# Kernel tuning notes

Hardware: AMD Instinct MI355X
Metric: run time of the kernel (lower is better)

Reference implementation:

```python
import jax, jax.numpy as jnp
import numpy as np

DT = 0.5
DX = 0.01
MU_UP = 4e-05
PAD = 3  # 7x7 kernel // 2

_LAP = np.array([[0, 0, 0, 2, 0, 0, 0],
                 [0, 0, 0, -27, 0, 0, 0],
                 [0, 0, 0, 270, 0, 0, 0],
                 [2, -27, 270, -980, 270, -27, 2],
                 [0, 0, 0, 270, 0, 0, 0],
                 [0, 0, 0, -27, 0, 0, 0],
                 [0, 0, 0, 2, 0, 0, 0]], dtype=np.float32)
LAP_W = jnp.asarray(_LAP / (DX * DX) / 180.0)[None, None]  # [1,1,7,7]


def _laplace(x):
    # x: [B,1,H,W]; circular padding then valid conv (matches padding_mode='circular')
    xp = jnp.pad(x, ((0, 0), (0, 0), (PAD, PAD), (PAD, PAD)), mode='wrap')
    return jax.lax.conv_general_dilated(xp, LAP_W, (1, 1), 'VALID',
                                        dimension_numbers=('NCHW', 'OIHW', 'NCHW'))


def setup_inputs() -> dict:
    key = jax.random.key(0)
    ks = jax.random.split(key, 7)
    h = jax.random.uniform(ks[0], (16, 2, 1024, 1024), dtype=jnp.float32)
    CA = jax.random.uniform(ks[1], (), dtype=jnp.float32) - 0.5  # ~ -rand()+0.5
    CB = jax.random.uniform(ks[2], (), dtype=jnp.float32) - 0.5
    NA = -jax.random.uniform(ks[3], (), dtype=jnp.float32)
    NB = jax.random.uniform(ks[4], (), dtype=jnp.float32)
    f = 0.1 * jax.random.uniform(ks[5], (), dtype=jnp.float32)
    k = 0.1 * jax.random.uniform(ks[6], (), dtype=jnp.float32)
    return {"h": h, "CA": CA, "CB": CB, "NA": NA, "NB": NB, "f": f, "k": k}


def reference(h, CA, CB, NA, NB, f, k):
    mu_u = MU_UP * jax.nn.sigmoid(CA)
    mu_v = MU_UP * jax.nn.sigmoid(CB)

    def f_rhs(u, v):
        uv2 = u * v * v
        f_u = mu_u * _laplace(u) + NA * uv2 + f * (1.0 - u)
        f_v = mu_v * _laplace(v) + NB * uv2 - (k + f) * v
        return f_u, f_v

    u0 = h[:, 0:1]
    v0 = h[:, 1:2]
    k1_u, k1_v = f_rhs(u0, v0)
    k2_u, k2_v = f_rhs(u0 + k1_u * (DT / 2.0), v0 + k1_v * (DT / 2.0))
    k3_u, k3_v = f_rhs(u0 + k2_u * (DT / 2.0), v0 + k2_v * (DT / 2.0))
    k4_u, k4_v = f_rhs(u0 + k3_u * DT, v0 + k3_v * DT)
    u_next = u0 + DT * (k1_u + 2.0 * k2_u + 2.0 * k3_u + k4_u) / 6.0
    v_next = v0 + DT * (k1_v + 2.0 * k2_v + 2.0 * k3_v + k4_v) / 6.0
    return jnp.concatenate((u_next, v_next), axis=1)
```

## Files before the change

### kernel.cpp

```cpp
#include <hip/hip_runtime.h>


typedef float f2 __attribute__((ext_vector_type(2)));

#define HROWS 64
#define NT    512
#define STEPS (HROWS + 24)

#define W0 ((-980.0f / 1e-4f) / 180.0f)
#define W1 ((  270.0f / 1e-4f) / 180.0f)
#define W2 (( -27.0f / 1e-4f) / 180.0f)
#define W3 ((   2.0f / 1e-4f) / 180.0f)

__device__ __forceinline__ f2 sp(float s) { f2 r; r.x = s; r.y = s; return r; }
__device__ __forceinline__ f2 pfma(float s, f2 a, f2 c) {
    return __builtin_elementwise_fma(sp(s), a, c);
}

__device__ __forceinline__ unsigned pk2(f2 a) {
    unsigned ua = __float_as_uint(a.x), ub = __float_as_uint(a.y);
    return ((ua + 0x8000u) >> 16) | ((ub + 0x8000u) & 0xffff0000u);
}
__device__ __forceinline__ float bhi(unsigned d) { return __uint_as_float(d); }
__device__ __forceinline__ float blo(unsigned d) { return __uint_as_float(d << 16); }

__device__ __forceinline__ void evalp7x(f2 w0, f2 w1, f2 w2, f2 w3, f2 w4,
                                        f2 w5, f2 w6, f2 m1, f2 p1,
                                        float am3, float bp3,
                                        f2& lap, f2& ctr)
{
    ctr = w3;
    f2 vp = pfma(W1, w2 + w4, pfma(W2, w1 + w5, sp(W3) * (w0 + w6)));
    f2 m1q; m1q.x = m1.y;  m1q.y = ctr.x;
    f2 p1q; p1q.x = ctr.y; p1q.y = p1.x;
    f2 m3q; m3q.x = am3;   m3q.y = m1.x;
    f2 p3q; p3q.x = p1.y;  p3q.y = bp3;
    f2 hp = pfma(W1, m1q + p1q, pfma(W2, m1 + p1, sp(W3) * (m3q + p3q)));
    lap = pfma(W0, ctr, hp + vp);
}

__global__ __launch_bounds__(NT, 1) void rcnn_rk4_march(
    const float* __restrict__ h,
    const float* __restrict__ pCA, const float* __restrict__ pCB,
    const float* __restrict__ pNA, const float* __restrict__ pNB,
    const float* __restrict__ pf,  const float* __restrict__ pk,
    float* __restrict__ out)
{
    __shared__ uint2 S[4][4][NT];

    const int tid = threadIdx.x;
    const int Y0  = blockIdx.x * HROWS;
    const int b   = blockIdx.z;

    const float NA = pNA[0], NB = pNB[0];
    const float ff = pf[0];
    const float kpf = pk[0] + pf[0];
    const float mu_u = 4e-5f / (1.0f + expf(-pCA[0]));
    const float mu_v = 4e-5f / (1.0f + expf(-pCB[0]));

    const size_t baseU = (size_t)b * 2u * 1048576u;
    const size_t baseV = baseU + 1048576u;
    const float* hU = h + baseU + 2 * tid;
    const float* hV = h + baseV + 2 * tid;
    float* oU = out + baseU + 2 * tid;
    float* oV = out + baseV + 2 * tid;

    const int xm2 = (tid - 2) & 511;
    const int xm1 = (tid - 1) & 511;
    const int xp1 = (tid + 1) & 511;
    const int xp2 = (tid + 2) & 511;

    f2 Uu[8], Uv[8], Du[8], Dv[8];
    f2 Y1u[8], Y1v[8], Y2u[8], Y2v[8], Y3u[8], Y3v[8];
    f2 ACu[8], ACv[8];

    const f2 z = sp(0.0f);
    #pragma unroll
    for (int j = 0; j < 8; ++j) {
        Uu[j]=z; Uv[j]=z; Du[j]=z; Dv[j]=z;
        Y1u[j]=z; Y1v[j]=z; Y2u[j]=z; Y2v[j]=z; Y3u[j]=z; Y3v[j]=z;
        ACu[j]=z; ACv[j]=z;
    }

    f2 pAu, pAv, pBu, pBv;
    {
        int r0 = (Y0 - 12) & 1023;
        int r1 = (Y0 - 11) & 1023;
        pAu = *(const f2*)(hU + (size_t)r0 * 1024);
        pAv = *(const f2*)(hV + (size_t)r0 * 1024);
        pBu = *(const f2*)(hU + (size_t)r1 * 1024);
        pBv = *(const f2*)(hV + (size_t)r1 * 1024);
    }

#define NBR(sidx, cc)                                                         \
      const uint2* Ls = &S[sidx][((cc)+2)&3][0];                              \
      uint2 m2d = Ls[xm2], m1d = Ls[xm1], p1d = Ls[xp1], p2d = Ls[xp2];       \
      f2 m1u; m1u.x = blo(m1d.x); m1u.y = bhi(m1d.x);                         \
      f2 p1u; p1u.x = blo(p1d.x); p1u.y = bhi(p1d.x);                         \
      f2 m1v; m1v.x = blo(m1d.y); m1v.y = bhi(m1d.y);                         \
      f2 p1v; p1v.x = blo(p1d.y); p1v.y = bhi(p1d.y);                         \
      float am3u = bhi(m2d.x), am3v = bhi(m2d.y);                             \
      float bp3u = blo(p2d.x), bp3v = blo(p2d.y);

#define STEP(c, G1, G2, G3, G4, tb_)                                          \
  {                                                                           \
    const int t_ = (tb_) + (c);                                               \
                             \
    Du[(c)&7] = Uu[((c)+3)&7]; Dv[(c)&7] = Uv[((c)+3)&7];                     \
                                             \
    Uu[(c)&7] = ((c)&1) ? pBu : pAu;                                          \
    Uv[(c)&7] = ((c)&1) ? pBv : pAv;                                          \
             \
    S[0][(c)&3][tid] = make_uint2(pk2(Uu[((c)+7)&7]), pk2(Uv[((c)+7)&7]));    \
                                             \
    {                                                                         \
      int yn = (Y0 - 10 + t_) & 1023;                                         \
      f2 au = *(const f2*)(hU + (size_t)yn * 1024);                           \
      f2 av = *(const f2*)(hV + (size_t)yn * 1024);                           \
      if ((c)&1) { pBu = au; pBv = av; } else { pAu = au; pAv = av; }         \
    }                                                                         \
    if (G1) {                                         \
      NBR(0, c)                                                               \
      f2 lU, cU, lV, cV;                                                      \
      evalp7x(Uu[((c)+2)&7], Uu[((c)+3)&7], Uu[((c)+4)&7], Uu[((c)+5)&7],     \
              Uu[((c)+6)&7], Uu[((c)+7)&7], Uu[(c)&7],                        \
              m1u, p1u, am3u, bp3u, lU, cU);                                  \
      evalp7x(Uv[((c)+2)&7], Uv[((c)+3)&7], Uv[((c)+4)&7], Uv[((c)+5)&7],     \
              Uv[((c)+6)&7], Uv[((c)+7)&7], Uv[(c)&7],                        \
              m1v, p1v, am3v, bp3v, lV, cV);                                  \
      f2 uv2 = cU * cV * cV;                                                  \
      f2 kU = pfma(mu_u, lU, pfma(NA, uv2, pfma(-ff, cU, sp(ff))));           \
      f2 kV = pfma(mu_v, lV, pfma(NB, uv2, sp(-kpf) * cV));                   \
      Y1u[(c)&7] = pfma(0.25f, kU, cU);                                       \
      Y1v[(c)&7] = pfma(0.25f, kV, cV);                                       \
      S[1][(c)&3][tid] = make_uint2(pk2(Y1u[((c)+7)&7]), pk2(Y1v[((c)+7)&7]));\
    }                                                                         \
    if (G2) {                               \
      NBR(1, c)                                                               \
      f2 lU, cU, lV, cV;                                                      \
      evalp7x(Y1u[((c)+2)&7], Y1u[((c)+3)&7], Y1u[((c)+4)&7], Y1u[((c)+5)&7], \
              Y1u[((c)+6)&7], Y1u[((c)+7)&7], Y1u[(c)&7],                     \
              m1u, p1u, am3u, bp3u, lU, cU);                                  \
      evalp7x(Y1v[((c)+2)&7], Y1v[((c)+3)&7], Y1v[((c)+4)&7], Y1v[((c)+5)&7], \
              Y1v[((c)+6)&7], Y1v[((c)+7)&7], Y1v[(c)&7],                     \
              m1v, p1v, am3v, bp3v, lV, cV);                                  \
      f2 uv2 = cU * cV * cV;                                                  \
      f2 kU = pfma(mu_u, lU, pfma(NA, uv2, pfma(-ff, cU, sp(ff))));           \
      f2 kV = pfma(mu_v, lV, pfma(NB, uv2, sp(-kpf) * cV));                   \
      f2 bu = Du[((c)+7)&7], bv = Dv[((c)+7)&7];                \
      f2 nu = pfma(0.25f, kU, bu), nv = pfma(0.25f, kV, bv);                  \
      Y2u[(c)&7] = nu; Y2v[(c)&7] = nv;                                       \
      f2 aU = pfma(4.0f, Y1u[((c)+5)&7], sp(8.0f) * nu);                      \
      f2 aV = pfma(4.0f, Y1v[((c)+5)&7], sp(8.0f) * nv);                      \
      ACu[(c)&7] = pfma(-4.0f, bu, aU);                                       \
      ACv[(c)&7] = pfma(-4.0f, bv, aV);                                       \
      S[2][(c)&3][tid] = make_uint2(pk2(Y2u[((c)+7)&7]), pk2(Y2v[((c)+7)&7]));\
    }                                                                         \
    if (G3) {                                         \
      NBR(2, c)                                                               \
      f2 lU, cU, lV, cV;                                                      \
      evalp7x(Y2u[((c)+2)&7], Y2u[((c)+3)&7], Y2u[((c)+4)&7], Y2u[((c)+5)&7], \
              Y2u[((c)+6)&7], Y2u[((c)+7)&7], Y2u[(c)&7],                     \
              m1u, p1u, am3u, bp3u, lU, cU);                                  \
      evalp7x(Y2v[((c)+2)&7], Y2v[((c)+3)&7], Y2v[((c)+4)&7], Y2v[((c)+5)&7], \
              Y2v[((c)+6)&7], Y2v[((c)+7)&7], Y2v[(c)&7],                     \
              m1v, p1v, am3v, bp3v, lV, cV);                                  \
      f2 uv2 = cU * cV * cV;                                                  \
      f2 kU = pfma(mu_u, lU, pfma(NA, uv2, pfma(-ff, cU, sp(ff))));           \
      f2 kV = pfma(mu_v, lV, pfma(NB, uv2, sp(-kpf) * cV));                   \
      Y3u[(c)&7] = pfma(0.5f, kU, Du[((c)+4)&7]);               \
      Y3v[(c)&7] = pfma(0.5f, kV, Dv[((c)+4)&7]);                             \
      S[3][(c)&3][tid] = make_uint2(pk2(Y3u[((c)+7)&7]), pk2(Y3v[((c)+7)&7]));\
    }                                                                         \
    if (G4) {                         \
      NBR(3, c)                                                               \
      f2 lU, cU4, lV, cV4;                                                    \
      evalp7x(Y3u[((c)+2)&7], Y3u[((c)+3)&7], Y3u[((c)+4)&7], Y3u[((c)+5)&7], \
              Y3u[((c)+6)&7], Y3u[((c)+7)&7], Y3u[(c)&7],                     \
              m1u, p1u, am3u, bp3u, lU, cU4);                                 \
      evalp7x(Y3v[((c)+2)&7], Y3v[((c)+3)&7], Y3v[((c)+4)&7], Y3v[((c)+5)&7], \
              Y3v[((c)+6)&7], Y3v[((c)+7)&7], Y3v[(c)&7],                     \
              m1v, p1v, am3v, bp3v, lV, cV4);                                 \
      f2 uv2 = cU4 * cV4 * cV4;                                               \
      f2 kU = pfma(mu_u, lU, pfma(NA, uv2, pfma(-ff, cU4, sp(ff))));          \
      f2 kV = pfma(mu_v, lV, pfma(NB, uv2, sp(-kpf) * cV4));                  \
      f2 sU = pfma(4.0f, cU4, kU) + ACu[((c)+2)&7];             \
      f2 sV = pfma(4.0f, cV4, kV) + ACv[((c)+2)&7];                           \
      f2 oUq = sp(1.0f / 12.0f) * sU;                                         \
      f2 oVq = sp(1.0f / 12.0f) * sV;                                         \
      int yS = Y0 + t_ - 24;                                                  \
      *(f2*)(oU + (size_t)yS * 1024) = oUq;                                   \
      *(f2*)(oV + (size_t)yS * 1024) = oVq;                                   \
    }                                                                         \
    if ((c) & 1) {                                                            \
      asm volatile("s_waitcnt lgkmcnt(0)" ::: "memory");                      \
      __builtin_amdgcn_s_barrier();                                           \
    }                                                                         \
  }

    STEP(0,0,0,0,0, 0) STEP(1,0,0,0,0, 0) STEP(2,0,0,0,0, 0) STEP(3,0,0,0,0, 0)
    STEP(4,0,0,0,0, 0) STEP(5,0,0,0,0, 0) STEP(6,1,0,0,0, 0) STEP(7,1,0,0,0, 0)

    STEP(0,1,0,0,0, 8) STEP(1,1,0,0,0, 8) STEP(2,1,0,0,0, 8) STEP(3,1,0,0,0, 8)
    STEP(4,1,1,0,0, 8) STEP(5,1,1,0,0, 8) STEP(6,1,1,0,0, 8) STEP(7,1,1,0,0, 8)

    STEP(0,1,1,0,0,16) STEP(1,1,1,0,0,16) STEP(2,1,1,1,0,16) STEP(3,1,1,1,0,16)
    STEP(4,1,1,1,0,16) STEP(5,1,1,1,0,16) STEP(6,1,1,1,0,16) STEP(7,1,1,1,0,16)

    #pragma unroll 1
    for (int tb = 24; tb < STEPS; tb += 8) {
        STEP(0,1,1,1,1,tb) STEP(1,1,1,1,1,tb) STEP(2,1,1,1,1,tb) STEP(3,1,1,1,1,tb)
        STEP(4,1,1,1,1,tb) STEP(5,1,1,1,1,tb) STEP(6,1,1,1,1,tb) STEP(7,1,1,1,1,tb)
    }
#undef STEP
#undef NBR
}

extern "C" void kernel_launch(void* const* d_in, const int* in_sizes, int n_in,
                              void* d_out, int out_size, void* d_ws, size_t ws_size,
                              hipStream_t stream) {
    const float* h   = (const float*)d_in[0];
    const float* pCA = (const float*)d_in[1];
    const float* pCB = (const float*)d_in[2];
    const float* pNA = (const float*)d_in[3];
    const float* pNB = (const float*)d_in[4];
    const float* pf  = (const float*)d_in[5];
    const float* pk  = (const float*)d_in[6];
    float* outp = (float*)d_out;

    dim3 grid(1024 / HROWS, 1, 16);
    dim3 block(NT);
    rcnn_rk4_march<<<grid, block, 0, stream>>>(h, pCA, pCB, pNA, pNB, pf, pk, outp);
}
```

Baseline: 104.1 us.

## Share neighbor columns via DPP and store fp32 halos in shared memory

```diff
diff --git a/kernel.cpp b/kernel.cpp
--- a/kernel.cpp
+++ b/kernel.cpp
@@ -2,6 +2,7 @@
 
 
 typedef float f2 __attribute__((ext_vector_type(2)));
+typedef float f4 __attribute__((ext_vector_type(4)));
 
 #define HROWS 64
 #define NT    512
@@ -12,17 +13,18 @@
 #define W2 (( -27.0f / 1e-4f) / 180.0f)
 #define W3 ((   2.0f / 1e-4f) / 180.0f)
 
+#define DPP_PAIR 0xB1
+
 __device__ __forceinline__ f2 sp(float s) { f2 r; r.x = s; r.y = s; return r; }
 __device__ __forceinline__ f2 pfma(float s, f2 a, f2 c) {
     return __builtin_elementwise_fma(sp(s), a, c);
 }
 
-__device__ __forceinline__ unsigned pk2(f2 a) {
-    unsigned ua = __float_as_uint(a.x), ub = __float_as_uint(a.y);
-    return ((ua + 0x8000u) >> 16) | ((ub + 0x8000u) & 0xffff0000u);
-}
-__device__ __forceinline__ float bhi(unsigned d) { return __uint_as_float(d); }
-__device__ __forceinline__ float blo(unsigned d) { return __uint_as_float(d << 16); }
+template<int C>
+__device__ __forceinline__ float dppf(float x) {
+    return __int_as_float(__builtin_amdgcn_update_dpp(
+        0, __float_as_int(x), C, 0xF, 0xF, false));
+}
 
 __device__ __forceinline__ void evalp7x(f2 w0, f2 w1, f2 w2, f2 w3, f2 w4,
                                         f2 w5, f2 w6, f2 m1, f2 p1,
@@ -46,7 +48,7 @@
     const float* __restrict__ pf,  const float* __restrict__ pk,
     float* __restrict__ out)
 {
-    __shared__ uint2 S[4][4][NT];
+    __shared__ f4 S[4][4][NT];
 
     const int tid = threadIdx.x;
     const int Y0  = blockIdx.x * HROWS;
@@ -65,10 +67,9 @@
     float* oU = out + baseU + 2 * tid;
     float* oV = out + baseV + 2 * tid;
 
-    const int xm2 = (tid - 2) & 511;
-    const int xm1 = (tid - 1) & 511;
-    const int xp1 = (tid + 1) & 511;
-    const int xp2 = (tid + 2) & 511;
+    const bool odd = (tid & 1);
+    const int ad1 = (tid + (odd ? 1 : -1)) & 511;
+    const int ad2 = (tid + (odd ? 2 : -2)) & 511;
 
     f2 Uu[8], Uv[8], Du[8], Dv[8];
     f2 Y1u[8], Y1v[8], Y2u[8], Y2v[8], Y3u[8], Y3v[8];
@@ -92,15 +93,21 @@
         pBv = *(const f2*)(hV + (size_t)r1 * 1024);
     }
 
-#define NBR(sidx, cc)                                                         \
-      const uint2* Ls = &S[sidx][((cc)+2)&3][0];                              \
-      uint2 m2d = Ls[xm2], m1d = Ls[xm1], p1d = Ls[xp1], p2d = Ls[xp2];       \
-      f2 m1u; m1u.x = blo(m1d.x); m1u.y = bhi(m1d.x);                         \
-      f2 p1u; p1u.x = blo(p1d.x); p1u.y = bhi(p1d.x);                         \
-      f2 m1v; m1v.x = blo(m1d.y); m1v.y = bhi(m1d.y);                         \
-      f2 p1v; p1v.x = blo(p1d.y); p1v.y = bhi(p1d.y);                         \
-      float am3u = bhi(m2d.x), am3v = bhi(m2d.y);                             \
-      float bp3u = blo(p2d.x), bp3v = blo(p2d.y);
+#define NBR(Wu_, Wv_, sidx, cc)                                               \
+      const f4* Ls = &S[sidx][((cc)+2)&3][0];                                 \
+      f4 Aq = Ls[ad1];                                                        \
+      f4 Bq = Ls[ad2];                                                        \
+      f2 w3u_ = Wu_[((cc)+5)&7], w3v_ = Wv_[((cc)+5)&7];                      \
+      f2 wpu; wpu.x = dppf<DPP_PAIR>(w3u_.x); wpu.y = dppf<DPP_PAIR>(w3u_.y); \
+      f2 wpv; wpv.x = dppf<DPP_PAIR>(w3v_.x); wpv.y = dppf<DPP_PAIR>(w3v_.y); \
+      float pAux = dppf<DPP_PAIR>(Aq.x), pAuy = dppf<DPP_PAIR>(Aq.y);         \
+      float pAvx = dppf<DPP_PAIR>(Aq.z), pAvy = dppf<DPP_PAIR>(Aq.w);         \
+      f2 Au_; Au_.x = Aq.x; Au_.y = Aq.y;                                     \
+      f2 Av_; Av_.x = Aq.z; Av_.y = Aq.w;                                     \
+      f2 m1u = odd ? wpu : Au_;  f2 p1u = odd ? Au_ : wpu;                    \
+      f2 m1v = odd ? wpv : Av_;  f2 p1v = odd ? Av_ : wpv;                    \
+      float am3u = odd ? pAuy : Bq.y,  bp3u = odd ? Bq.x : pAux;              \
+      float am3v = odd ? pAvy : Bq.w,  bp3v = odd ? Bq.z : pAvx;
 
 #define STEP(c, G1, G2, G3, G4, tb_)                                          \
   {                                                                           \
@@ -110,8 +117,9 @@
                                              \
     Uu[(c)&7] = ((c)&1) ? pBu : pAu;                                          \
     Uv[(c)&7] = ((c)&1) ? pBv : pAv;                                          \
-             \
-    S[0][(c)&3][tid] = make_uint2(pk2(Uu[((c)+7)&7]), pk2(Uv[((c)+7)&7]));    \
+                          \
+    S[0][(c)&3][tid] = __builtin_shufflevector(Uu[((c)+7)&7], Uv[((c)+7)&7],  \
+                                               0, 1, 2, 3);                   \
                                              \
     {                                                                         \
       int yn = (Y0 - 10 + t_) & 1023;                                         \
@@ -120,7 +128,7 @@
       if ((c)&1) { pBu = au; pBv = av; } else { pAu = au; pAv = av; }         \
     }                                                                         \
     if (G1) {                                         \
-      NBR(0, c)                                                               \
+      NBR(Uu, Uv, 0, c)                                                       \
       f2 lU, cU, lV, cV;                                                      \
       evalp7x(Uu[((c)+2)&7], Uu[((c)+3)&7], Uu[((c)+4)&7], Uu[((c)+5)&7],     \
               Uu[((c)+6)&7], Uu[((c)+7)&7], Uu[(c)&7],                        \
@@ -133,10 +141,11 @@
       f2 kV = pfma(mu_v, lV, pfma(NB, uv2, sp(-kpf) * cV));                   \
       Y1u[(c)&7] = pfma(0.25f, kU, cU);                                       \
       Y1v[(c)&7] = pfma(0.25f, kV, cV);                                       \
-      S[1][(c)&3][tid] = make_uint2(pk2(Y1u[((c)+7)&7]), pk2(Y1v[((c)+7)&7]));\
+      S[1][(c)&3][tid] = __builtin_shufflevector(Y1u[((c)+7)&7],              \
+                                                 Y1v[((c)+7)&7], 0, 1, 2, 3); \
     }                                                                         \
     if (G2) {                               \
-      NBR(1, c)                                                               \
+      NBR(Y1u, Y1v, 1, c)                                                     \
       f2 lU, cU, lV, cV;                                                      \
       evalp7x(Y1u[((c)+2)&7], Y1u[((c)+3)&7], Y1u[((c)+4)&7], Y1u[((c)+5)&7], \
               Y1u[((c)+6)&7], Y1u[((c)+7)&7], Y1u[(c)&7],                     \
@@ -154,10 +163,11 @@
       f2 aV = pfma(4.0f, Y1v[((c)+5)&7], sp(8.0f) * nv);                      \
       ACu[(c)&7] = pfma(-4.0f, bu, aU);                                       \
       ACv[(c)&7] = pfma(-4.0f, bv, aV);                                       \
-      S[2][(c)&3][tid] = make_uint2(pk2(Y2u[((c)+7)&7]), pk2(Y2v[((c)+7)&7]));\
+      S[2][(c)&3][tid] = __builtin_shufflevector(Y2u[((c)+7)&7],              \
+                                                 Y2v[((c)+7)&7], 0, 1, 2, 3); \
     }                                                                         \
     if (G3) {                                         \
-      NBR(2, c)                                                               \
+      NBR(Y2u, Y2v, 2, c)                                                     \
       f2 lU, cU, lV, cV;                                                      \
       evalp7x(Y2u[((c)+2)&7], Y2u[((c)+3)&7], Y2u[((c)+4)&7], Y2u[((c)+5)&7], \
               Y2u[((c)+6)&7], Y2u[((c)+7)&7], Y2u[(c)&7],                     \
@@ -170,10 +180,11 @@
       f2 kV = pfma(mu_v, lV, pfma(NB, uv2, sp(-kpf) * cV));                   \
       Y3u[(c)&7] = pfma(0.5f, kU, Du[((c)+4)&7]);               \
       Y3v[(c)&7] = pfma(0.5f, kV, Dv[((c)+4)&7]);                             \
-      S[3][(c)&3][tid] = make_uint2(pk2(Y3u[((c)+7)&7]), pk2(Y3v[((c)+7)&7]));\
+      S[3][(c)&3][tid] = __builtin_shufflevector(Y3u[((c)+7)&7],              \
+                                                 Y3v[((c)+7)&7], 0, 1, 2, 3); \
     }                                                                         \
     if (G4) {                         \
-      NBR(3, c)                                                               \
+      NBR(Y3u, Y3v, 3, c)                                                     \
       f2 lU, cU4, lV, cV4;                                                    \
       evalp7x(Y3u[((c)+2)&7], Y3u[((c)+3)&7], Y3u[((c)+4)&7], Y3u[((c)+5)&7], \
               Y3u[((c)+6)&7], Y3u[((c)+7)&7], Y3u[(c)&7],                     \
```

Measured after the change: 103.5 us. Within noise of the previous version (-0.5%).
